# Performance work log

Measured on AMD Instinct MI355X. Metric: run time of the kernel, lower is better.

Reference implementation:

```python
import jax, jax.numpy as jnp
import numpy as np

INDIM, HID, OUTDIM, T = 28, 128, 10, 28

def setup_inputs() -> dict:
    key = jax.random.key(0)
    ks = jax.random.split(key, 7)
    B = 65536
    bound1 = 1.0 / np.sqrt(INDIM)
    bound2 = 1.0 / np.sqrt(2 * HID)
    bound3 = 1.0 / np.sqrt(HID)
    return {
        "x": jax.random.normal(ks[0], (B, 784), dtype=jnp.float32),
        "W1": jax.random.uniform(ks[1], (INDIM, HID), jnp.float32, -bound1, bound1),
        "b1": jax.random.uniform(ks[2], (HID,), jnp.float32, -bound1, bound1),
        "W2": jax.random.uniform(ks[3], (2 * HID, HID), jnp.float32, -bound2, bound2),
        "b2": jax.random.uniform(ks[4], (HID,), jnp.float32, -bound2, bound2),
        "W3": jax.random.uniform(ks[5], (HID, OUTDIM), jnp.float32, -bound3, bound3),
        "b3": jax.random.uniform(ks[6], (OUTDIM,), jnp.float32, -bound3, bound3),
    }

def reference(x, W1, b1, W2, b2, W3, b3):
    B = x.shape[0]
    # (B, 784) -> (T, B, 28): scan over the 28 rows of each image
    rows = jnp.transpose(x.reshape(B, T, INDIM), (1, 0, 2))
    # W2 split: first HID rows multiply linear1 output, last HID rows multiply hidden state
    W2a, W2b = W2[:HID], W2[HID:]

    def step(h, row):
        t = row @ W1 + b1                      # (B, HID)
        h_new = jax.nn.relu(t @ W2a + h @ W2b + b2)  # concat(t, h) @ W2 == t@W2a + h@W2b
        return h_new, None

    h0 = jnp.zeros((B, HID), dtype=x.dtype)
    h_final, _ = jax.lax.scan(step, h0, rows)
    return h_final @ W3 + b3
```

## Files before the change

### kernel.cpp

```cpp
#include <hip/hip_runtime.h>

#define BTOT 65536
#define TST  28
#define PACK_DW 100
#define WXL_OFF 12800

typedef __attribute__((ext_vector_type(8))) short bf16x8;
typedef __attribute__((ext_vector_type(4))) float f32x4;
typedef __attribute__((ext_vector_type(2))) unsigned int u32x2;

__device__ __forceinline__ unsigned int f2bf(float f) {
    unsigned u = __float_as_uint(f);
    u += 0x7fff + ((u >> 16) & 1);
    return u >> 16;
}
__device__ __forceinline__ unsigned int pk2bf(float a, float b) {
    return f2bf(a) | (f2bf(b) << 16);
}
__device__ __forceinline__ bf16x8 cvt8(f32x4 a, f32x4 b) {
    union { unsigned int u[4]; bf16x8 v; } r;
    asm("v_cvt_pk_bf16_f32 %0, %1, %2" : "=v"(r.u[0]) : "v"(a[0]), "v"(a[1]));
    asm("v_cvt_pk_bf16_f32 %0, %1, %2" : "=v"(r.u[1]) : "v"(a[2]), "v"(a[3]));
    asm("v_cvt_pk_bf16_f32 %0, %1, %2" : "=v"(r.u[2]) : "v"(b[0]), "v"(b[1]));
    asm("v_cvt_pk_bf16_f32 %0, %1, %2" : "=v"(r.u[3]) : "v"(b[2]), "v"(b[3]));
    return r.v;
}

__global__ void pack1(const float* __restrict__ W1, const float* __restrict__ b1,
                      const float* __restrict__ W2, const float* __restrict__ b2,
                      const float* __restrict__ W3, const float* __restrict__ b3,
                      unsigned int* __restrict__ ws) {
    float* WxL = (float*)(ws + WXL_OFF);
    const int bid = blockIdx.x, tid = threadIdx.x;
    if (bid < 29) {
        const int k = bid, n = tid;
        float s = 0.f;
        if (k < 28) {
            for (int m = 0; m < 128; ++m) s += W1[k * 128 + m] * W2[m * 128 + n];
        } else {
            s = b2[n];
            for (int m = 0; m < 128; ++m) s += b1[m] * W2[m * 128 + n];
        }
        WxL[k * 128 + n] = s;
        if (k == 28) { WxL[29*128+n] = 0.f; WxL[30*128+n] = 0.f; WxL[31*128+n] = 0.f; }
    } else if (bid == 29) {
        if (tid < 64) {
            const int lr = tid & 15, kh = tid >> 4;
            for (int p = 0; p < 2; ++p) {
                unsigned int* P = ws + (p * 64 + tid) * PACK_DW;
                for (int kk = 0; kk < 4; ++kk)
                    for (int t = 0; t < 4; ++t)
                        for (int jd = 0; jd < 4; ++jd) {
                            const int k = 128 + kk * 32 + kh * 8 + jd * 2;
                            const int n = p * 64 + t * 16 + lr;
                            P[(kk * 4 + t) * 4 + jd] =
                                pk2bf(W2[k * 128 + n], W2[(k + 1) * 128 + n]);
                        }
            }
        }
    } else {
        if (tid < 64) {
            const int lr = tid & 15, kh = tid >> 4;
            unsigned int* P = ws + tid * PACK_DW;
            for (int kk = 0; kk < 4; ++kk)
                for (int jd = 0; jd < 4; ++jd) {
                    const int k = kk * 32 + kh * 8 + jd * 2;
                    float lo = (lr < 10) ? W3[k * 10 + lr] : 0.f;
                    float hi = (lr < 10) ? W3[(k + 1) * 10 + lr] : 0.f;
                    P[80 + kk * 4 + jd] = pk2bf(lo, hi);
                }
            for (int j = 0; j < 4; ++j) {
                const int o = kh * 4 + j;
                P[96 + j] = __float_as_uint((o < 10) ? b3[o] : 0.f);
            }
        }
    }
}

__global__ void pack2(unsigned int* __restrict__ ws) {
    const int tid = threadIdx.x;
    if (tid < 64) {
        const float* WxL = (const float*)(ws + WXL_OFF);
        const int lr = tid & 15, kh = tid >> 4;
        for (int p = 0; p < 2; ++p) {
            unsigned int* P = ws + (p * 64 + tid) * PACK_DW;
            for (int t = 0; t < 4; ++t)
                for (int jd = 0; jd < 4; ++jd) {
                    const int k = kh * 8 + jd * 2, n = p * 64 + t * 16 + lr;
                    P[64 + t * 4 + jd] = pk2bf(WxL[k * 128 + n], WxL[(k + 1) * 128 + n]);
                }
        }
    }
}

__global__ __launch_bounds__(256, 3) void rnn_kernel(
    const float* __restrict__ x, const unsigned int* __restrict__ wsPack,
    float* __restrict__ out)
{
    __shared__ __align__(16) short Hs[2][2][16][136];
    const int tid = threadIdx.x;
    const int w = tid >> 6, lane = tid & 63, lr = lane & 15, kh = lane >> 4;
    const int g = w >> 1, p = w & 1;
    const int r0 = blockIdx.x * 32 + g * 16;

    const unsigned int* P = wsPack + (p * 64 + lane) * PACK_DW;
    bf16x8 w2b[4][4], wx[4];
    #pragma unroll
    for (int kk = 0; kk < 4; ++kk)
        #pragma unroll
        for (int t = 0; t < 4; ++t)
            w2b[kk][t] = *(const bf16x8*)(P + (kk * 4 + t) * 4);
    #pragma unroll
    for (int t = 0; t < 4; ++t) wx[t] = *(const bf16x8*)(P + 64 + t * 4);

    unsigned int* hz = (unsigned int*)&Hs[0][0][0][0];
    #pragma unroll
    for (int i = 0; i < 17; ++i) hz[tid + i * 256] = 0u;
    __syncthreads();

    const float* xr = x + (size_t)(r0 + lr) * 784 + 8 * kh;
    f32x4 xa = *(const f32x4*)xr;
    f32x4 xc = (kh < 3) ? *(const f32x4*)(xr + 4) : (f32x4){1.f, 0.f, 0.f, 0.f};
    bf16x8 xb = cvt8(xa, xc);
    const f32x4 z4 = {0.f, 0.f, 0.f, 0.f};

    int cur = 0;
    for (int t = 0; t < TST; ++t) {
        f32x4 acc[4];
        #pragma unroll
        for (int t4 = 0; t4 < 4; ++t4)
            acc[t4] = __builtin_amdgcn_mfma_f32_16x16x32_bf16(wx[t4], xb, z4, 0, 0, 0);
        f32x4 na, nc;
        if (t + 1 < TST) {
            const float* xp = xr + (t + 1) * 28;
            na = *(const f32x4*)xp;
            nc = (kh < 3) ? *(const f32x4*)(xp + 4) : (f32x4){1.f, 0.f, 0.f, 0.f};
        }
        bf16x8 hbv[4];
        #pragma unroll
        for (int kk = 0; kk < 4; ++kk)
            hbv[kk] = *(const bf16x8*)&Hs[g][cur][lr][kk * 32 + kh * 8];
        #pragma unroll
        for (int kk = 0; kk < 4; ++kk)
            #pragma unroll
            for (int t4 = 0; t4 < 4; ++t4)
                acc[t4] = __builtin_amdgcn_mfma_f32_16x16x32_bf16(w2b[kk][t4], hbv[kk], acc[t4], 0, 0, 0);
        #pragma unroll
        for (int t4 = 0; t4 < 4; ++t4) {
            f32x4 v = acc[t4];
            v[0] = fmaxf(v[0], 0.f); v[1] = fmaxf(v[1], 0.f);
            v[2] = fmaxf(v[2], 0.f); v[3] = fmaxf(v[3], 0.f);
            unsigned lo, hi;
            asm("v_cvt_pk_bf16_f32 %0, %1, %2" : "=v"(lo) : "v"(v[0]), "v"(v[1]));
            asm("v_cvt_pk_bf16_f32 %0, %1, %2" : "=v"(hi) : "v"(v[2]), "v"(v[3]));
            u32x2 st = {lo, hi};
            *(u32x2*)&Hs[g][cur ^ 1][lr][p * 64 + t4 * 16 + kh * 4] = st;
        }
        if (t + 1 < TST) xb = cvt8(na, nc);
        __syncthreads();
        cur ^= 1;
    }

    if (p == 0) {
        bf16x8 w3f[4];
        #pragma unroll
        for (int kk = 0; kk < 4; ++kk) w3f[kk] = *(const bf16x8*)(P + 80 + kk * 4);
        const float* bp = (const float*)(P + 96);
        f32x4 accO = {bp[0], bp[1], bp[2], bp[3]};
        #pragma unroll
        for (int kk = 0; kk < 4; ++kk) {
            bf16x8 hb = *(const bf16x8*)&Hs[g][cur][lr][kk * 32 + kh * 8];
            accO = __builtin_amdgcn_mfma_f32_16x16x32_bf16(w3f[kk], hb, accO, 0, 0, 0);
        }
        float* op = out + (size_t)(r0 + lr) * 10 + kh * 4;
        #pragma unroll
        for (int j = 0; j < 4; ++j)
            if (kh * 4 + j < 10) op[j] = accO[j];
    }
}

extern "C" void kernel_launch(void* const* d_in, const int* in_sizes, int n_in,
                              void* d_out, int out_size, void* d_ws, size_t ws_size,
                              hipStream_t stream) {
    const float* x  = (const float*)d_in[0];
    const float* W1 = (const float*)d_in[1];
    const float* b1 = (const float*)d_in[2];
    const float* W2 = (const float*)d_in[3];
    const float* b2 = (const float*)d_in[4];
    const float* W3 = (const float*)d_in[5];
    const float* b3 = (const float*)d_in[6];
    unsigned int* ws = (unsigned int*)d_ws;

    pack1<<<31, 128, 0, stream>>>(W1, b1, W2, b2, W3, b3, ws);
    pack2<<<1, 64, 0, stream>>>(ws);
    rnn_kernel<<<BTOT / 32, 256, 0, stream>>>(x, ws, (float*)d_out);
}
```

Before: 80.38 us.

## Process two 16-row groups per wave to interleave independent recurrences

Each block now has 2 waves instead of 4, and every wave handles both 16-row batch groups. It runs two independent MFMA chains per timestep, which gives instruction-level parallelism that hides MFMA and LDS latency. Each wave keeps its W2b and Wx registers resident while doing twice the work per weight load. The final projection is now split across both waves by group, so W3 and b3 are packed for both lane sets. This raises register pressure and halves the waves per block, which could reduce occupancy-based latency hiding.

```diff
diff --git a/kernel.cpp b/kernel.cpp
--- a/kernel.cpp
+++ b/kernel.cpp
@@ -61,17 +61,19 @@
     } else {
         if (tid < 64) {
             const int lr = tid & 15, kh = tid >> 4;
-            unsigned int* P = ws + tid * PACK_DW;
-            for (int kk = 0; kk < 4; ++kk)
-                for (int jd = 0; jd < 4; ++jd) {
-                    const int k = kk * 32 + kh * 8 + jd * 2;
-                    float lo = (lr < 10) ? W3[k * 10 + lr] : 0.f;
-                    float hi = (lr < 10) ? W3[(k + 1) * 10 + lr] : 0.f;
-                    P[80 + kk * 4 + jd] = pk2bf(lo, hi);
+            for (int p = 0; p < 2; ++p) {
+                unsigned int* P = ws + (p * 64 + tid) * PACK_DW;
+                for (int kk = 0; kk < 4; ++kk)
+                    for (int jd = 0; jd < 4; ++jd) {
+                        const int k = kk * 32 + kh * 8 + jd * 2;
+                        float lo = (lr < 10) ? W3[k * 10 + lr] : 0.f;
+                        float hi = (lr < 10) ? W3[(k + 1) * 10 + lr] : 0.f;
+                        P[80 + kk * 4 + jd] = pk2bf(lo, hi);
+                    }
+                for (int j = 0; j < 4; ++j) {
+                    const int o = kh * 4 + j;
+                    P[96 + j] = __float_as_uint((o < 10) ? b3[o] : 0.f);
                 }
-            for (int j = 0; j < 4; ++j) {
-                const int o = kh * 4 + j;
-                P[96 + j] = __float_as_uint((o < 10) ? b3[o] : 0.f);
             }
         }
     }
@@ -93,15 +95,14 @@
     }
 }
 
-__global__ __launch_bounds__(256, 3) void rnn_kernel(
+__global__ __launch_bounds__(128, 3) void rnn_kernel(
     const float* __restrict__ x, const unsigned int* __restrict__ wsPack,
     float* __restrict__ out)
 {
     __shared__ __align__(16) short Hs[2][2][16][136];
     const int tid = threadIdx.x;
-    const int w = tid >> 6, lane = tid & 63, lr = lane & 15, kh = lane >> 4;
-    const int g = w >> 1, p = w & 1;
-    const int r0 = blockIdx.x * 32 + g * 16;
+    const int p = tid >> 6, lane = tid & 63, lr = lane & 15, kh = lane >> 4;
+    const int r0 = blockIdx.x * 32;
 
     const unsigned int* P = wsPack + (p * 64 + lane) * PACK_DW;
     bf16x8 w2b[4][4], wx[4];
@@ -115,36 +116,55 @@
 
     unsigned int* hz = (unsigned int*)&Hs[0][0][0][0];
     #pragma unroll
-    for (int i = 0; i < 17; ++i) hz[tid + i * 256] = 0u;
+    for (int g = 0; g < 2; ++g)
+        #pragma unroll
+        for (int i = 0; i < 9; ++i) {
+            const int idx = tid + i * 128;
+            if (idx < 1088) hz[g * 2176 + idx] = 0u;
+        }
     __syncthreads();
 
-    const float* xr = x + (size_t)(r0 + lr) * 784 + 8 * kh;
-    f32x4 xa = *(const f32x4*)xr;
-    f32x4 xc = (kh < 3) ? *(const f32x4*)(xr + 4) : (f32x4){1.f, 0.f, 0.f, 0.f};
-    bf16x8 xb = cvt8(xa, xc);
+    const f32x4 onec = {1.f, 0.f, 0.f, 0.f};
+    const float* xrA = x + (size_t)(r0 + lr) * 784 + 8 * kh;
+    const float* xrB = xrA + 16 * 784;
+    f32x4 a0 = *(const f32x4*)xrA;
+    f32x4 c0 = (kh < 3) ? *(const f32x4*)(xrA + 4) : onec;
+    bf16x8 xbA = cvt8(a0, c0);
+    a0 = *(const f32x4*)xrB;
+    c0 = (kh < 3) ? *(const f32x4*)(xrB + 4) : onec;
+    bf16x8 xbB = cvt8(a0, c0);
     const f32x4 z4 = {0.f, 0.f, 0.f, 0.f};
 
     int cur = 0;
     for (int t = 0; t < TST; ++t) {
+        bf16x8 hbvA[4], hbvB[4];
+        #pragma unroll
+        for (int kk = 0; kk < 4; ++kk)
+            hbvA[kk] = *(const bf16x8*)&Hs[0][cur][lr][kk * 32 + kh * 8];
+        #pragma unroll
+        for (int kk = 0; kk < 4; ++kk)
+            hbvB[kk] = *(const bf16x8*)&Hs[1][cur][lr][kk * 32 + kh * 8];
+
+        f32x4 naA, ncA, naB, ncB;
+        const bool pf = (t + 1 < TST);
+        if (pf) {
+            const float* xp = xrA + (t + 1) * 28;
+            naA = *(const f32x4*)xp;
+            ncA = (kh < 3) ? *(const f32x4*)(xp + 4) : onec;
+            xp = xrB + (t + 1) * 28;
+            naB = *(const f32x4*)xp;
+            ncB = (kh < 3) ? *(const f32x4*)(xp + 4) : onec;
+        }
+
         f32x4 acc[4];
         #pragma unroll
         for (int t4 = 0; t4 < 4; ++t4)
-            acc[t4] = __builtin_amdgcn_mfma_f32_16x16x32_bf16(wx[t4], xb, z4, 0, 0, 0);
-        f32x4 na, nc;
-        if (t + 1 < TST) {
-            const float* xp = xr + (t + 1) * 28;
-            na = *(const f32x4*)xp;
-            nc = (kh < 3) ? *(const f32x4*)(xp + 4) : (f32x4){1.f, 0.f, 0.f, 0.f};
-        }
-        bf16x8 hbv[4];
-        #pragma unroll
-        for (int kk = 0; kk < 4; ++kk)
-            hbv[kk] = *(const bf16x8*)&Hs[g][cur][lr][kk * 32 + kh * 8];
+            acc[t4] = __builtin_amdgcn_mfma_f32_16x16x32_bf16(wx[t4], xbA, z4, 0, 0, 0);
         #pragma unroll
         for (int kk = 0; kk < 4; ++kk)
             #pragma unroll
             for (int t4 = 0; t4 < 4; ++t4)
-                acc[t4] = __builtin_amdgcn_mfma_f32_16x16x32_bf16(w2b[kk][t4], hbv[kk], acc[t4], 0, 0, 0);
+                acc[t4] = __builtin_amdgcn_mfma_f32_16x16x32_bf16(w2b[kk][t4], hbvA[kk], acc[t4], 0, 0, 0);
         #pragma unroll
         for (int t4 = 0; t4 < 4; ++t4) {
             f32x4 v = acc[t4];
@@ -154,29 +174,49 @@
             asm("v_cvt_pk_bf16_f32 %0, %1, %2" : "=v"(lo) : "v"(v[0]), "v"(v[1]));
             asm("v_cvt_pk_bf16_f32 %0, %1, %2" : "=v"(hi) : "v"(v[2]), "v"(v[3]));
             u32x2 st = {lo, hi};
-            *(u32x2*)&Hs[g][cur ^ 1][lr][p * 64 + t4 * 16 + kh * 4] = st;
-        }
-        if (t + 1 < TST) xb = cvt8(na, nc);
+            *(u32x2*)&Hs[0][cur ^ 1][lr][p * 64 + t4 * 16 + kh * 4] = st;
+        }
+        if (pf) xbA = cvt8(naA, ncA);
+
+        #pragma unroll
+        for (int t4 = 0; t4 < 4; ++t4)
+            acc[t4] = __builtin_amdgcn_mfma_f32_16x16x32_bf16(wx[t4], xbB, z4, 0, 0, 0);
+        #pragma unroll
+        for (int kk = 0; kk < 4; ++kk)
+            #pragma unroll
+            for (int t4 = 0; t4 < 4; ++t4)
+                acc[t4] = __builtin_amdgcn_mfma_f32_16x16x32_bf16(w2b[kk][t4], hbvB[kk], acc[t4], 0, 0, 0);
+        #pragma unroll
+        for (int t4 = 0; t4 < 4; ++t4) {
+            f32x4 v = acc[t4];
+            v[0] = fmaxf(v[0], 0.f); v[1] = fmaxf(v[1], 0.f);
+            v[2] = fmaxf(v[2], 0.f); v[3] = fmaxf(v[3], 0.f);
+            unsigned lo, hi;
+            asm("v_cvt_pk_bf16_f32 %0, %1, %2" : "=v"(lo) : "v"(v[0]), "v"(v[1]));
+            asm("v_cvt_pk_bf16_f32 %0, %1, %2" : "=v"(hi) : "v"(v[2]), "v"(v[3]));
+            u32x2 st = {lo, hi};
+            *(u32x2*)&Hs[1][cur ^ 1][lr][p * 64 + t4 * 16 + kh * 4] = st;
+        }
+        if (pf) xbB = cvt8(naB, ncB);
+
         __syncthreads();
         cur ^= 1;
     }
 
-    if (p == 0) {
-        bf16x8 w3f[4];
-        #pragma unroll
-        for (int kk = 0; kk < 4; ++kk) w3f[kk] = *(const bf16x8*)(P + 80 + kk * 4);
-        const float* bp = (const float*)(P + 96);
-        f32x4 accO = {bp[0], bp[1], bp[2], bp[3]};
-        #pragma unroll
-        for (int kk = 0; kk < 4; ++kk) {
-            bf16x8 hb = *(const bf16x8*)&Hs[g][cur][lr][kk * 32 + kh * 8];
-            accO = __builtin_amdgcn_mfma_f32_16x16x32_bf16(w3f[kk], hb, accO, 0, 0, 0);
-        }
-        float* op = out + (size_t)(r0 + lr) * 10 + kh * 4;
-        #pragma unroll
-        for (int j = 0; j < 4; ++j)
-            if (kh * 4 + j < 10) op[j] = accO[j];
-    }
+    bf16x8 w3f[4];
+    #pragma unroll
+    for (int kk = 0; kk < 4; ++kk) w3f[kk] = *(const bf16x8*)(P + 80 + kk * 4);
+    const float* bp = (const float*)(P + 96);
+    f32x4 accO = {bp[0], bp[1], bp[2], bp[3]};
+    #pragma unroll
+    for (int kk = 0; kk < 4; ++kk) {
+        bf16x8 hb = *(const bf16x8*)&Hs[p][cur][lr][kk * 32 + kh * 8];
+        accO = __builtin_amdgcn_mfma_f32_16x16x32_bf16(w3f[kk], hb, accO, 0, 0, 0);
+    }
+    float* op = out + (size_t)(r0 + p * 16 + lr) * 10 + kh * 4;
+    #pragma unroll
+    for (int j = 0; j < 4; ++j)
+        if (kh * 4 + j < 10) op[j] = accO[j];
 }
 
 extern "C" void kernel_launch(void* const* d_in, const int* in_sizes, int n_in,
@@ -193,5 +233,5 @@
 
     pack1<<<31, 128, 0, stream>>>(W1, b1, W2, b2, W3, b3, ws);
     pack2<<<1, 64, 0, stream>>>(ws);
-    rnn_kernel<<<BTOT / 32, 256, 0, stream>>>(x, ws, (float*)d_out);
-}
+    rnn_kernel<<<BTOT / 32, 128, 0, stream>>>(x, ws, (float*)d_out);
+}
```

Measured after the change: 88.85 us. 1.11x slower.
